# Optimization experiments

Hardware: AMD Instinct MI355X
Metric: run time of the kernel (lower is better)

Reference implementation:

```python
import jax, jax.numpy as jnp
import numpy as np

N, D, K = 65536, 4096, 16
LN_EPS = 1e-5
SN_EPS = 1e-12
MIN_NORM = 1e-15


def setup_inputs() -> dict:
    key = jax.random.key(0)
    k1, k2, k3, k4 = jax.random.split(key, 4)
    return {
        "x": jax.random.normal(k1, (N, D), dtype=jnp.float32),
        "gamma": jnp.ones((D,), dtype=jnp.float32),
        "beta": jnp.zeros((D,), dtype=jnp.float32),
        "W": jax.random.normal(k2, (K, D), dtype=jnp.float32) * 0.02,
        "u": jax.random.normal(k3, (K,), dtype=jnp.float32),
        "log_scale": jnp.float32(-2.0),
    }


def _l2_normalize(v, eps=SN_EPS):
    return v / (jnp.linalg.norm(v) + eps)


def reference(x, gamma, beta, W, u, log_scale):
    # LayerNorm over last dim
    mean = jnp.mean(x, axis=-1, keepdims=True)
    var = jnp.mean(jnp.square(x - mean), axis=-1, keepdims=True)
    xn = (x - mean) * jax.lax.rsqrt(var + LN_EPS) * gamma + beta

    # spectral norm of W: one power iteration (torch spectral_norm forward)
    v = _l2_normalize(W.T @ u)           # [D]
    u_new = _l2_normalize(W @ v)         # [K]
    sigma = u_new @ (W @ v)              # scalar, top singular value estimate
    W_sn = W / sigma

    # linear (no bias) + learned scale
    vout = xn @ W_sn.T                   # [N, K]
    scale = jax.nn.sigmoid(log_scale) * 0.5
    vout = vout * scale

    # Poincare ball expmap0 with c=1: tanh(||v||) * v / ||v||
    vnorm = jnp.maximum(jnp.linalg.norm(vout, axis=-1, keepdims=True), MIN_NORM)
    return jnp.tanh(vnorm) * vout / vnorm
```

## Files before the change

kernel.cpp:

```cpp
#include <hip/hip_runtime.h>
#include <hip/hip_bf16.h>


#define ND 4096
#define NK 16
#define NROWS 65536

using f32x4  = __attribute__((ext_vector_type(4))) float;
using bf16x8 = __attribute__((ext_vector_type(8))) short;

#define GWB_OFF  0u
#define SC_OFF   131072u

__device__ __forceinline__ unsigned short f2bf(float f) {
    union { __hip_bfloat16 h; unsigned short u; } cv;
    cv.h = __float2bfloat16(f);
    return cv.u;
}

__global__ __launch_bounds__(1024) void prep(
    const float* __restrict__ W, const float* __restrict__ gamma,
    const float* __restrict__ beta, const float* __restrict__ u,
    const float* __restrict__ log_scale,
    unsigned short* __restrict__ ws_gwb, float* __restrict__ sc)
{
    const int tid = threadIdx.x;
    const int lane = tid & 63, wid = tid >> 6;
    __shared__ float t_sh[ND];
    __shared__ float wred[16][34];
    __shared__ float tot[34];

    float uu[NK];
#pragma unroll
    for (int k = 0; k < NK; ++k) uu[k] = u[k];

    const int d0 = tid * 4;
    const f32x4 g4 = *(const f32x4*)(gamma + d0);
    const f32x4 b4 = *(const f32x4*)(beta + d0);

    f32x4 t4 = {0.f, 0.f, 0.f, 0.f};
    float G[NK], B[NK];
    const int c8 = tid >> 1;
    const int j0 = (tid & 1) * 4;
#pragma unroll
    for (int k = 0; k < NK; ++k) {
        const f32x4 w4 = *(const f32x4*)(W + k * ND + d0);
        t4[0] = fmaf(w4[0], uu[k], t4[0]);
        t4[1] = fmaf(w4[1], uu[k], t4[1]);
        t4[2] = fmaf(w4[2], uu[k], t4[2]);
        t4[3] = fmaf(w4[3], uu[k], t4[3]);
        const float gw0 = g4[0]*w4[0], gw1 = g4[1]*w4[1], gw2 = g4[2]*w4[2], gw3 = g4[3]*w4[3];
        G[k] = (gw0 + gw1) + (gw2 + gw3);
        B[k] = (b4[0]*w4[0] + b4[1]*w4[1]) + (b4[2]*w4[2] + b4[3]*w4[3]);
        ushort4 st;
        st.x = f2bf(gw0); st.y = f2bf(gw1); st.z = f2bf(gw2); st.w = f2bf(gw3);
        *(ushort4*)(ws_gwb + (c8 * NK + k) * 8 + j0) = st;
    }
    *(f32x4*)(t_sh + d0) = t4;
    float nt2 = (t4[0]*t4[0] + t4[1]*t4[1]) + (t4[2]*t4[2] + t4[3]*t4[3]);
#pragma unroll
    for (int m = 1; m < 64; m <<= 1) {
        nt2 += __shfl_xor(nt2, m);
#pragma unroll
        for (int k = 0; k < NK; ++k) {
            G[k] += __shfl_xor(G[k], m);
            B[k] += __shfl_xor(B[k], m);
        }
    }
    if (lane == 0) {
        wred[wid][0] = nt2;
#pragma unroll
        for (int k = 0; k < NK; ++k) { wred[wid][1 + k] = G[k]; wred[wid][17 + k] = B[k]; }
    }
    __syncthreads();
    if (tid < 33) {
        float s = 0.f;
        for (int w = 0; w < 16; ++w) s += wred[w][tid];
        tot[tid] = s;
    }
    __syncthreads();
    const float inv_nt = 1.0f / (sqrtf(tot[0]) + 1e-12f);
    f32x4 tv = *(const f32x4*)(t_sh + d0);
    tv[0] *= inv_nt; tv[1] *= inv_nt; tv[2] *= inv_nt; tv[3] *= inv_nt;
    float sp[NK];
#pragma unroll
    for (int k = 0; k < NK; ++k) {
        const f32x4 w4 = *(const f32x4*)(W + k * ND + d0);
        sp[k] = (w4[0]*tv[0] + w4[1]*tv[1]) + (w4[2]*tv[2] + w4[3]*tv[3]);
    }
#pragma unroll
    for (int m = 1; m < 64; m <<= 1) {
#pragma unroll
        for (int k = 0; k < NK; ++k) sp[k] += __shfl_xor(sp[k], m);
    }
    __syncthreads();
    if (lane == 0) {
#pragma unroll
        for (int k = 0; k < NK; ++k) wred[wid][k] = sp[k];
    }
    __syncthreads();
    if (tid == 0) {
        float ns2 = 0.f;
        for (int k = 0; k < NK; ++k) {
            float s = 0.f;
            for (int w = 0; w < 16; ++w) s += wred[w][k];
            ns2 += s * s;
        }
        const float sigma = ns2 / (sqrtf(ns2) + 1e-12f);
        const float scale = 0.5f / (1.0f + expf(-log_scale[0]));
        sc[0] = scale / sigma;
#pragma unroll
        for (int k = 0; k < NK; ++k) { sc[1 + k] = tot[1 + k]; sc[17 + k] = tot[17 + k]; }
    }
}

__global__ __launch_bounds__(1024, 4) void hyp_main(
    const float* __restrict__ x, const unsigned short* __restrict__ gwb_g,
    const float* __restrict__ sc, float* __restrict__ out)
{
    __shared__ unsigned short gwb[ND * NK];

    const int lane = threadIdx.x & 63;
    const int wid  = threadIdx.x >> 6;
    const int tile = (blockIdx.x << 4) + wid;
    const int lr = lane & 15;
    const int lc = lane >> 4;

    const float* xp = x + (size_t)(tile * 16 + lr) * ND + lc * 8;
    const unsigned short* lp = gwb + lane * 8;

    f32x4 xa = __builtin_nontemporal_load((const f32x4*)xp);
    f32x4 xb = __builtin_nontemporal_load((const f32x4*)(xp + 4));

    {
        const uint4* src = (const uint4*)gwb_g;
        uint4* dst = (uint4*)gwb;
#pragma unroll
        for (int i = 0; i < 8; ++i)
            dst[threadIdx.x + i * 1024] = src[threadIdx.x + i * 1024];
    }
    __syncthreads();

    const float coef = sc[0];
    const float gk = sc[1 + lr];
    const float bk = sc[17 + lr];

    f32x4 acc = {0.f, 0.f, 0.f, 0.f};
    float s1 = 0.f, s2 = 0.f;

#define PROCESS(XA, XB, CC) do {                                          \
        bf16x8 afrag;                                                     \
        afrag[0] = (short)f2bf(XA[0]); afrag[1] = (short)f2bf(XA[1]);     \
        afrag[2] = (short)f2bf(XA[2]); afrag[3] = (short)f2bf(XA[3]);     \
        afrag[4] = (short)f2bf(XB[0]); afrag[5] = (short)f2bf(XB[1]);     \
        afrag[6] = (short)f2bf(XB[2]); afrag[7] = (short)f2bf(XB[3]);     \
        s1 += ((XA[0] + XA[1]) + (XA[2] + XA[3]))                         \
            + ((XB[0] + XB[1]) + (XB[2] + XB[3]));                        \
        s2 = fmaf(XA[0], XA[0], s2); s2 = fmaf(XA[1], XA[1], s2);         \
        s2 = fmaf(XA[2], XA[2], s2); s2 = fmaf(XA[3], XA[3], s2);         \
        s2 = fmaf(XB[0], XB[0], s2); s2 = fmaf(XB[1], XB[1], s2);         \
        s2 = fmaf(XB[2], XB[2], s2); s2 = fmaf(XB[3], XB[3], s2);         \
        bf16x8 bfrag = *(const bf16x8*)(lp + (CC) * 16);                  \
        acc = __builtin_amdgcn_mfma_f32_16x16x32_bf16(afrag, bfrag, acc, 0, 0, 0); \
    } while (0)

#pragma unroll 4
    for (int c = 0; c < ND - 32; c += 32) {
        f32x4 na = __builtin_nontemporal_load((const f32x4*)(xp + c + 32));
        f32x4 nb = __builtin_nontemporal_load((const f32x4*)(xp + c + 36));
        PROCESS(xa, xb, c);
        xa = na; xb = nb;
    }
    PROCESS(xa, xb, ND - 32);
#undef PROCESS

    s1 += __shfl_xor(s1, 16); s1 += __shfl_xor(s1, 32);
    s2 += __shfl_xor(s2, 16); s2 += __shfl_xor(s2, 32);
    const float mean = s1 * (1.0f / ND);
    const float var  = s2 * (1.0f / ND) - mean * mean;
    const float rstd = rsqrtf(var + 1e-5f);

    float vout[4];
#pragma unroll
    for (int j = 0; j < 4; ++j) {
        const int r = lc * 4 + j;
        const float m_r  = __shfl(mean, r);
        const float rs_r = __shfl(rstd, r);
        vout[j] = coef * (fmaf(-m_r, gk, acc[j]) * rs_r + bk);
    }

    float nsq[4];
#pragma unroll
    for (int j = 0; j < 4; ++j) nsq[j] = vout[j] * vout[j];
#pragma unroll
    for (int m = 1; m < 16; m <<= 1) {
#pragma unroll
        for (int j = 0; j < 4; ++j) nsq[j] += __shfl_xor(nsq[j], m);
    }

#pragma unroll
    for (int j = 0; j < 4; ++j) {
        float nv = sqrtf(nsq[j]);
        nv = fmaxf(nv, 1e-15f);
        const float fac = tanhf(nv) / nv;
        __builtin_nontemporal_store(vout[j] * fac,
            out + (size_t)(tile * 16 + lc * 4 + j) * NK + lr);
    }
}

extern "C" void kernel_launch(void* const* d_in, const int* in_sizes, int n_in,
                              void* d_out, int out_size, void* d_ws, size_t ws_size,
                              hipStream_t stream) {
    const float* x     = (const float*)d_in[0];
    const float* gamma = (const float*)d_in[1];
    const float* beta  = (const float*)d_in[2];
    const float* W     = (const float*)d_in[3];
    const float* u     = (const float*)d_in[4];
    const float* ls    = (const float*)d_in[5];

    char* ws = (char*)d_ws;
    unsigned short* ws_gwb = (unsigned short*)(ws + GWB_OFF);
    float* sc      = (float*)(ws + SC_OFF);
    float* out     = (float*)d_out;

    prep<<<1, 1024, 0, stream>>>(W, gamma, beta, u, ls, ws_gwb, sc);
    hyp_main<<<256, 1024, 0, stream>>>(x, ws_gwb, sc, out);
}
```

Before: 213.5 us.

## Fuse spectral-norm prep into main kernel with staggered per-tile K-chunk order

Removes the separate single-block prep kernel and its global workspace round-trip. Every block now recomputes the power iteration, the gamma*W bf16 fragments and the bias terms straight into LDS. The x loads use a new lane-to-column mapping, and each wave starts its K sweep at a pseudo-random chunk offset, likely to spread concurrent DRAM traffic across channels. The explicit register prefetch is dropped and plain loads and stores replace the nontemporal ones. The cost is redundant per-block W reads and the reduction work at each block's start.

```diff
diff --git a/kernel.cpp b/kernel.cpp
--- a/kernel.cpp
+++ b/kernel.cpp
@@ -8,9 +8,6 @@
 
 using f32x4  = __attribute__((ext_vector_type(4))) float;
 using bf16x8 = __attribute__((ext_vector_type(8))) short;
-
-#define GWB_OFF  0u
-#define SC_OFF   131072u
 
 __device__ __forceinline__ unsigned short f2bf(float f) {
     union { __hip_bfloat16 h; unsigned short u; } cv;
@@ -18,137 +15,131 @@
     return cv.u;
 }
 
-__global__ __launch_bounds__(1024) void prep(
-    const float* __restrict__ W, const float* __restrict__ gamma,
-    const float* __restrict__ beta, const float* __restrict__ u,
-    const float* __restrict__ log_scale,
-    unsigned short* __restrict__ ws_gwb, float* __restrict__ sc)
+__global__ __launch_bounds__(1024, 4) void hyp_fused(
+    const float* __restrict__ x, const float* __restrict__ W,
+    const float* __restrict__ gamma, const float* __restrict__ beta,
+    const float* __restrict__ u, const float* __restrict__ log_scale,
+    float* __restrict__ out)
 {
-    const int tid = threadIdx.x;
-    const int lane = tid & 63, wid = tid >> 6;
+    __shared__ unsigned short gwb[ND * NK];
     __shared__ float t_sh[ND];
     __shared__ float wred[16][34];
-    __shared__ float tot[34];
-
-    float uu[NK];
-#pragma unroll
-    for (int k = 0; k < NK; ++k) uu[k] = u[k];
-
-    const int d0 = tid * 4;
-    const f32x4 g4 = *(const f32x4*)(gamma + d0);
-    const f32x4 b4 = *(const f32x4*)(beta + d0);
-
-    f32x4 t4 = {0.f, 0.f, 0.f, 0.f};
-    float G[NK], B[NK];
-    const int c8 = tid >> 1;
-    const int j0 = (tid & 1) * 4;
-#pragma unroll
-    for (int k = 0; k < NK; ++k) {
-        const f32x4 w4 = *(const f32x4*)(W + k * ND + d0);
-        t4[0] = fmaf(w4[0], uu[k], t4[0]);
-        t4[1] = fmaf(w4[1], uu[k], t4[1]);
-        t4[2] = fmaf(w4[2], uu[k], t4[2]);
-        t4[3] = fmaf(w4[3], uu[k], t4[3]);
-        const float gw0 = g4[0]*w4[0], gw1 = g4[1]*w4[1], gw2 = g4[2]*w4[2], gw3 = g4[3]*w4[3];
-        G[k] = (gw0 + gw1) + (gw2 + gw3);
-        B[k] = (b4[0]*w4[0] + b4[1]*w4[1]) + (b4[2]*w4[2] + b4[3]*w4[3]);
-        ushort4 st;
-        st.x = f2bf(gw0); st.y = f2bf(gw1); st.z = f2bf(gw2); st.w = f2bf(gw3);
-        *(ushort4*)(ws_gwb + (c8 * NK + k) * 8 + j0) = st;
-    }
-    *(f32x4*)(t_sh + d0) = t4;
-    float nt2 = (t4[0]*t4[0] + t4[1]*t4[1]) + (t4[2]*t4[2] + t4[3]*t4[3]);
-#pragma unroll
-    for (int m = 1; m < 64; m <<= 1) {
-        nt2 += __shfl_xor(nt2, m);
-#pragma unroll
-        for (int k = 0; k < NK; ++k) {
-            G[k] += __shfl_xor(G[k], m);
-            B[k] += __shfl_xor(B[k], m);
-        }
-    }
-    if (lane == 0) {
-        wred[wid][0] = nt2;
-#pragma unroll
-        for (int k = 0; k < NK; ++k) { wred[wid][1 + k] = G[k]; wred[wid][17 + k] = B[k]; }
-    }
-    __syncthreads();
-    if (tid < 33) {
-        float s = 0.f;
-        for (int w = 0; w < 16; ++w) s += wred[w][tid];
-        tot[tid] = s;
-    }
-    __syncthreads();
-    const float inv_nt = 1.0f / (sqrtf(tot[0]) + 1e-12f);
-    f32x4 tv = *(const f32x4*)(t_sh + d0);
-    tv[0] *= inv_nt; tv[1] *= inv_nt; tv[2] *= inv_nt; tv[3] *= inv_nt;
-    float sp[NK];
-#pragma unroll
-    for (int k = 0; k < NK; ++k) {
-        const f32x4 w4 = *(const f32x4*)(W + k * ND + d0);
-        sp[k] = (w4[0]*tv[0] + w4[1]*tv[1]) + (w4[2]*tv[2] + w4[3]*tv[3]);
-    }
-#pragma unroll
-    for (int m = 1; m < 64; m <<= 1) {
-#pragma unroll
-        for (int k = 0; k < NK; ++k) sp[k] += __shfl_xor(sp[k], m);
-    }
-    __syncthreads();
-    if (lane == 0) {
-#pragma unroll
-        for (int k = 0; k < NK; ++k) wred[wid][k] = sp[k];
-    }
-    __syncthreads();
-    if (tid == 0) {
-        float ns2 = 0.f;
-        for (int k = 0; k < NK; ++k) {
-            float s = 0.f;
-            for (int w = 0; w < 16; ++w) s += wred[w][k];
-            ns2 += s * s;
-        }
-        const float sigma = ns2 / (sqrtf(ns2) + 1e-12f);
-        const float scale = 0.5f / (1.0f + expf(-log_scale[0]));
-        sc[0] = scale / sigma;
-#pragma unroll
-        for (int k = 0; k < NK; ++k) { sc[1 + k] = tot[1 + k]; sc[17 + k] = tot[17 + k]; }
-    }
-}
-
-__global__ __launch_bounds__(1024, 4) void hyp_main(
-    const float* __restrict__ x, const unsigned short* __restrict__ gwb_g,
-    const float* __restrict__ sc, float* __restrict__ out)
-{
-    __shared__ unsigned short gwb[ND * NK];
-
-    const int lane = threadIdx.x & 63;
-    const int wid  = threadIdx.x >> 6;
+    __shared__ float scl[34];
+
+    const int tid  = threadIdx.x;
+    const int lane = tid & 63;
+    const int wid  = tid >> 6;
     const int tile = (blockIdx.x << 4) + wid;
     const int lr = lane & 15;
     const int lc = lane >> 4;
 
-    const float* xp = x + (size_t)(tile * 16 + lr) * ND + lc * 8;
+    const float* xp = x + (size_t)(tile * 16 + lr) * ND + lc * 4;
     const unsigned short* lp = gwb + lane * 8;
-
-    f32x4 xa = __builtin_nontemporal_load((const f32x4*)xp);
-    f32x4 xb = __builtin_nontemporal_load((const f32x4*)(xp + 4));
+    const int start = (tile * 53) & 127;
+
+    const f32x4 xa0 = *(const f32x4*)(xp + start * 32);
+    const f32x4 xb0 = *(const f32x4*)(xp + start * 32 + 16);
 
     {
-        const uint4* src = (const uint4*)gwb_g;
-        uint4* dst = (uint4*)gwb;
-#pragma unroll
-        for (int i = 0; i < 8; ++i)
-            dst[threadIdx.x + i * 1024] = src[threadIdx.x + i * 1024];
-    }
-    __syncthreads();
-
-    const float coef = sc[0];
-    const float gk = sc[1 + lr];
-    const float bk = sc[17 + lr];
+        float uu[NK];
+#pragma unroll
+        for (int k = 0; k < NK; ++k) uu[k] = u[k];
+
+        const int d0 = tid * 4;
+        const f32x4 g4 = *(const f32x4*)(gamma + d0);
+        const f32x4 b4 = *(const f32x4*)(beta + d0);
+
+        const int s_i  = d0 >> 5;
+        const int wq   = d0 & 31;
+        const int lc_w = (wq >> 2) & 3;
+        const int j0   = (wq >> 4) << 2;
+        const int base = s_i * 512 + lc_w * 128 + j0;
+
+        f32x4 t4 = {0.f, 0.f, 0.f, 0.f};
+        float G[NK], B[NK];
+#pragma unroll 4
+        for (int k = 0; k < NK; ++k) {
+            const f32x4 w4 = *(const f32x4*)(W + k * ND + d0);
+            t4[0] = fmaf(w4[0], uu[k], t4[0]);
+            t4[1] = fmaf(w4[1], uu[k], t4[1]);
+            t4[2] = fmaf(w4[2], uu[k], t4[2]);
+            t4[3] = fmaf(w4[3], uu[k], t4[3]);
+            const float gw0 = g4[0]*w4[0], gw1 = g4[1]*w4[1];
+            const float gw2 = g4[2]*w4[2], gw3 = g4[3]*w4[3];
+            G[k] = (gw0 + gw1) + (gw2 + gw3);
+            B[k] = (b4[0]*w4[0] + b4[1]*w4[1]) + (b4[2]*w4[2] + b4[3]*w4[3]);
+            ushort4 st;
+            st.x = f2bf(gw0); st.y = f2bf(gw1); st.z = f2bf(gw2); st.w = f2bf(gw3);
+            *(ushort4*)(gwb + base + k * 8) = st;
+        }
+        *(f32x4*)(t_sh + d0) = t4;
+
+        float nt2 = (t4[0]*t4[0] + t4[1]*t4[1]) + (t4[2]*t4[2] + t4[3]*t4[3]);
+#pragma unroll
+        for (int m = 1; m < 64; m <<= 1) {
+            nt2 += __shfl_xor(nt2, m);
+#pragma unroll
+            for (int k = 0; k < NK; ++k) {
+                G[k] += __shfl_xor(G[k], m);
+                B[k] += __shfl_xor(B[k], m);
+            }
+        }
+        if (lane == 0) {
+            wred[wid][0] = nt2;
+#pragma unroll
+            for (int k = 0; k < NK; ++k) { wred[wid][1 + k] = G[k]; wred[wid][17 + k] = B[k]; }
+        }
+        __syncthreads();
+        if (tid < 33) {
+            float s = 0.f;
+#pragma unroll
+            for (int w = 0; w < 16; ++w) s += wred[w][tid];
+            scl[tid] = s;
+        }
+        __syncthreads();
+
+        const float inv_nt = 1.0f / (sqrtf(scl[0]) + 1e-12f);
+        f32x4 tv = *(const f32x4*)(t_sh + d0);
+        tv[0] *= inv_nt; tv[1] *= inv_nt; tv[2] *= inv_nt; tv[3] *= inv_nt;
+        float sp[NK];
+#pragma unroll 4
+        for (int k = 0; k < NK; ++k) {
+            const f32x4 w4 = *(const f32x4*)(W + k * ND + d0);
+            sp[k] = (w4[0]*tv[0] + w4[1]*tv[1]) + (w4[2]*tv[2] + w4[3]*tv[3]);
+        }
+#pragma unroll
+        for (int m = 1; m < 64; m <<= 1) {
+#pragma unroll
+            for (int k = 0; k < NK; ++k) sp[k] += __shfl_xor(sp[k], m);
+        }
+        __syncthreads();
+        if (lane == 0) {
+#pragma unroll
+            for (int k = 0; k < NK; ++k) wred[wid][k] = sp[k];
+        }
+        __syncthreads();
+        if (tid == 0) {
+            float ns2 = 0.f;
+            for (int k = 0; k < NK; ++k) {
+                float s = 0.f;
+                for (int w = 0; w < 16; ++w) s += wred[w][k];
+                ns2 += s * s;
+            }
+            const float sigma = ns2 / (sqrtf(ns2) + 1e-12f);
+            const float scale = 0.5f / (1.0f + expf(-log_scale[0]));
+            scl[0] = scale / sigma;
+        }
+        __syncthreads();
+    }
+
+    const float coef = scl[0];
+    const float gk = scl[1 + lr];
+    const float bk = scl[17 + lr];
 
     f32x4 acc = {0.f, 0.f, 0.f, 0.f};
     float s1 = 0.f, s2 = 0.f;
 
-#define PROCESS(XA, XB, CC) do {                                          \
+#define PROC_BODY(XA, XB, SS) do {                                        \
         bf16x8 afrag;                                                     \
         afrag[0] = (short)f2bf(XA[0]); afrag[1] = (short)f2bf(XA[1]);     \
         afrag[2] = (short)f2bf(XA[2]); afrag[3] = (short)f2bf(XA[3]);     \
@@ -160,19 +151,23 @@
         s2 = fmaf(XA[2], XA[2], s2); s2 = fmaf(XA[3], XA[3], s2);         \
         s2 = fmaf(XB[0], XB[0], s2); s2 = fmaf(XB[1], XB[1], s2);         \
         s2 = fmaf(XB[2], XB[2], s2); s2 = fmaf(XB[3], XB[3], s2);         \
-        bf16x8 bfrag = *(const bf16x8*)(lp + (CC) * 16);                  \
+        bf16x8 bfrag = *(const bf16x8*)(lp + (SS) * 512);                 \
         acc = __builtin_amdgcn_mfma_f32_16x16x32_bf16(afrag, bfrag, acc, 0, 0, 0); \
     } while (0)
 
-#pragma unroll 4
-    for (int c = 0; c < ND - 32; c += 32) {
-        f32x4 na = __builtin_nontemporal_load((const f32x4*)(xp + c + 32));
-        f32x4 nb = __builtin_nontemporal_load((const f32x4*)(xp + c + 36));
-        PROCESS(xa, xb, c);
-        xa = na; xb = nb;
-    }
-    PROCESS(xa, xb, ND - 32);
+#define PROCESS(SS) do {                                                  \
+        f32x4 xa = *(const f32x4*)(xp + (SS) * 32);                       \
+        f32x4 xb = *(const f32x4*)(xp + (SS) * 32 + 16);                  \
+        PROC_BODY(xa, xb, SS);                                            \
+    } while (0)
+
+    PROC_BODY(xa0, xb0, start);
+#pragma unroll 4
+    for (int s = start + 1; s < 128; ++s) PROCESS(s);
+#pragma unroll 4
+    for (int s = 0; s < start; ++s) PROCESS(s);
 #undef PROCESS
+#undef PROC_BODY
 
     s1 += __shfl_xor(s1, 16); s1 += __shfl_xor(s1, 32);
     s2 += __shfl_xor(s2, 16); s2 += __shfl_xor(s2, 32);
@@ -203,8 +198,7 @@
         float nv = sqrtf(nsq[j]);
         nv = fmaxf(nv, 1e-15f);
         const float fac = tanhf(nv) / nv;
-        __builtin_nontemporal_store(vout[j] * fac,
-            out + (size_t)(tile * 16 + lc * 4 + j) * NK + lr);
+        out[(size_t)(tile * 16 + lc * 4 + j) * NK + lr] = vout[j] * fac;
     }
 }
 
@@ -217,12 +211,7 @@
     const float* W     = (const float*)d_in[3];
     const float* u     = (const float*)d_in[4];
     const float* ls    = (const float*)d_in[5];
-
-    char* ws = (char*)d_ws;
-    unsigned short* ws_gwb = (unsigned short*)(ws + GWB_OFF);
-    float* sc      = (float*)(ws + SC_OFF);
-    float* out     = (float*)d_out;
-
-    prep<<<1, 1024, 0, stream>>>(W, gamma, beta, u, ls, ws_gwb, sc);
-    hyp_main<<<256, 1024, 0, stream>>>(x, ws_gwb, sc, out);
+    float* out = (float*)d_out;
+
+    hyp_fused<<<256, 1024, 0, stream>>>(x, W, gamma, beta, u, ls, out);
 }
```

Result: faster. 207.5 us (-2.8%).
